# Performance work log

Measured on AMD Instinct MI355X. Metric: run time of the kernel, lower is better.

Reference implementation:

```python
import jax, jax.numpy as jnp
import numpy as np
import math

B, Q_LEN, PAST, HID = 1, 1024, 3072, 4096
NH, NKV, HD = 32, 8, 128
KV_LEN = PAST + Q_LEN
ROPE_THETA = 10000.0


def setup_inputs() -> dict:
    key = jax.random.key(0)
    ks = jax.random.split(key, 8)
    s = 0.02
    hidden_states = jax.random.normal(ks[0], (B, Q_LEN, HID), jnp.float32)
    # additive causal mask with KV cache offset: query i attends keys j <= PAST + i
    i = jnp.arange(Q_LEN)[:, None]
    j = jnp.arange(KV_LEN)[None, :]
    attention_mask = jnp.where(j <= PAST + i, 0.0, -1e9).astype(jnp.float32)[None, None]
    position_ids = (jnp.arange(Q_LEN, dtype=jnp.int64) + PAST)[None, :]
    past_k = jax.random.normal(ks[1], (B, NKV, PAST, HD), jnp.float32)
    past_v = jax.random.normal(ks[2], (B, NKV, PAST, HD), jnp.float32)
    Wq = jax.random.normal(ks[3], (NH * HD, HID), jnp.float32) * s
    Wk = jax.random.normal(ks[4], (NKV * HD, HID), jnp.float32) * s
    Wv = jax.random.normal(ks[5], (NKV * HD, HID), jnp.float32) * s
    Wo = jax.random.normal(ks[6], (HID, NH * HD), jnp.float32) * s
    return {"hidden_states": hidden_states, "attention_mask": attention_mask,
            "position_ids": position_ids, "past_k": past_k, "past_v": past_v,
            "Wq": Wq, "Wk": Wk, "Wv": Wv, "Wo": Wo}


def _rope_tables(seq_len, head_dim, dtype):
    inv_freq = 1.0 / (ROPE_THETA ** (jnp.arange(0, head_dim, 2, dtype=jnp.float32) / head_dim))
    t = jnp.arange(seq_len, dtype=jnp.float32)
    freqs = jnp.outer(t, inv_freq)            # [seq, hd/2]
    emb = jnp.concatenate([freqs, freqs], -1)  # [seq, hd]
    return jnp.cos(emb).astype(dtype), jnp.sin(emb).astype(dtype)


def _rotate_half(x):
    x1, x2 = jnp.split(x, 2, axis=-1)
    return jnp.concatenate([-x2, x1], axis=-1)


def reference(hidden_states, attention_mask, position_ids, past_k, past_v, Wq, Wk, Wv, Wo):
    bsz, q_len, _ = hidden_states.shape
    q = (hidden_states @ Wq.T).reshape(bsz, q_len, NH, HD).transpose(0, 2, 1, 3)
    k = (hidden_states @ Wk.T).reshape(bsz, q_len, NKV, HD).transpose(0, 2, 1, 3)
    v = (hidden_states @ Wv.T).reshape(bsz, q_len, NKV, HD).transpose(0, 2, 1, 3)

    kv_seq_len = q_len + past_k.shape[2]
    cos_t, sin_t = _rope_tables(kv_seq_len, HD, q.dtype)
    cos = cos_t[position_ids][:, None]  # [b,1,q,hd]
    sin = sin_t[position_ids][:, None]
    q = q * cos + _rotate_half(q) * sin
    k = k * cos + _rotate_half(k) * sin

    k = jnp.concatenate([past_k, k], axis=2)  # [b,nkv,kv,hd]
    v = jnp.concatenate([past_v, v], axis=2)
    n_rep = NH // NKV
    k = jnp.repeat(k, n_rep, axis=1)  # GQA repeat_kv -> [b,nh,kv,hd]
    v = jnp.repeat(v, n_rep, axis=1)

    scores = jnp.einsum('bhqd,bhkd->bhqk', q, k) / math.sqrt(HD)
    scores = scores + attention_mask
    weights = jax.nn.softmax(scores.astype(jnp.float32), axis=-1).astype(q.dtype)
    attn = jnp.einsum('bhqk,bhkd->bhqd', weights, v)
    attn = attn.transpose(0, 2, 1, 3).reshape(bsz, q_len, NH * HD)
    return attn @ Wo.T
```

## Files before the change

### kernel.cpp

```cpp
#include <hip/hip_runtime.h>

#define QLEN 1024
#define PASTN 3072
#define KVLEN 4096
#define HIDN 4096
#define NHEAD 32
#define NKVH 8
#define HDIM 128
#define NQKVC 6144

typedef unsigned short u16;
typedef __bf16 bf16x8 __attribute__((ext_vector_type(8)));
typedef float f32x4 __attribute__((ext_vector_type(4)));
typedef float f32x16 __attribute__((ext_vector_type(16)));
typedef u16 us8 __attribute__((ext_vector_type(8)));
typedef u16 us4 __attribute__((ext_vector_type(4)));

__device__ __forceinline__ u16 f2bf(float x) {
  unsigned u = __builtin_bit_cast(unsigned, x);
  u += 0x7fffu + ((u >> 16) & 1u);
  return (u16)(u >> 16);
}
__device__ __forceinline__ float bf2f(u16 b) {
  return __builtin_bit_cast(float, (unsigned)b << 16);
}

#define GLL16(gp, lp) __builtin_amdgcn_global_load_lds( \
    (const __attribute__((address_space(1))) void*)(gp), \
    (__attribute__((address_space(3))) void*)(lp), 16, 0, 0)

__global__ __launch_bounds__(256) void cvt5_kernel(const float* __restrict__ hid,
                                                   const float* __restrict__ wq,
                                                   const float* __restrict__ wk,
                                                   const float* __restrict__ wv,
                                                   const float* __restrict__ woin,
                                                   u16* __restrict__ hb,
                                                   u16* __restrict__ wb,
                                                   u16* __restrict__ wob) {
  const int blk = blockIdx.x;
  const float* src;
  u16* dst;
  int off;
  if (blk < 4096)       { src = hid;  dst = hb;                       off = blk; }
  else if (blk < 20480) { src = wq;   dst = wb;                       off = blk - 4096; }
  else if (blk < 24576) { src = wk;   dst = wb + (size_t)4096 * HIDN; off = blk - 20480; }
  else if (blk < 28672) { src = wv;   dst = wb + (size_t)5120 * HIDN; off = blk - 24576; }
  else                  { src = woin; dst = wob;                      off = blk - 28672; }
  const int i = off * 1024 + threadIdx.x * 4;
  float4 f = *(const float4*)(src + i);
  ushort4 o = make_ushort4(f2bf(f.x), f2bf(f.y), f2bf(f.z), f2bf(f.w));
  *(ushort4*)(dst + i) = o;
}

__device__ __forceinline__ void storeC(float* p, float v) { *p = v; }
__device__ __forceinline__ void storeC(u16* p, float v) { *p = f2bf(v); }

template <typename CT>
__global__ __launch_bounds__(256) void gemm_bt(const u16* __restrict__ A,
                                               const u16* __restrict__ B,
                                               CT* __restrict__ C, int M, int N, int K) {
  __shared__ u16 Alds[2][128 * 32];
  __shared__ u16 Blds[2][128 * 32];
  const int tid = threadIdx.x, wid = tid >> 6, lane = tid & 63;
  const int m0 = blockIdx.y * 128, n0 = blockIdx.x * 128;
  const int wm = (wid >> 1) * 64, wn = (wid & 1) * 64;
  const int l15 = lane & 15, l4 = lane >> 4;
  const int srow = lane >> 2;
  const int scol = ((lane & 3) ^ ((lane >> 3) & 3)) * 8;
  f32x4 acc[4][4] = {};
  auto stage = [&](int buf, int kt) {
#pragma unroll
    for (int i = 0; i < 2; ++i) {
      const int c = wid * 2 + i;
      const int row = c * 16 + srow;
      GLL16(A + (size_t)(m0 + row) * K + kt + scol, &Alds[buf][c * 512]);
      GLL16(B + (size_t)(n0 + row) * K + kt + scol, &Blds[buf][c * 512]);
    }
  };
  stage(0, 0);
  __syncthreads();
  int cur = 0;
  for (int kt = 0; kt < K; kt += 32) {
    if (kt + 32 < K) stage(cur ^ 1, kt + 32);
    bf16x8 a[4], b[4];
#pragma unroll
    for (int i = 0; i < 4; ++i) {
      const int R = wm + i * 16 + l15;
      const int slot = l4 ^ ((R >> 1) & 3);
      a[i] = *(const bf16x8*)&Alds[cur][R * 32 + slot * 8];
    }
#pragma unroll
    for (int j = 0; j < 4; ++j) {
      const int R = wn + j * 16 + l15;
      const int slot = l4 ^ ((R >> 1) & 3);
      b[j] = *(const bf16x8*)&Blds[cur][R * 32 + slot * 8];
    }
#pragma unroll
    for (int i = 0; i < 4; ++i)
#pragma unroll
      for (int j = 0; j < 4; ++j)
        acc[i][j] = __builtin_amdgcn_mfma_f32_16x16x32_bf16(a[i], b[j], acc[i][j], 0, 0, 0);
    __syncthreads();
    cur ^= 1;
  }
#pragma unroll
  for (int i = 0; i < 4; ++i)
#pragma unroll
    for (int j = 0; j < 4; ++j) {
      int row = m0 + wm + i * 16 + l4 * 4;
      int col = n0 + wn + j * 16 + l15;
#pragma unroll
      for (int r = 0; r < 4; ++r) storeC(&C[(size_t)(row + r) * N + col], acc[i][j][r]);
    }
}

__global__ __launch_bounds__(256) void rope_q_kernel(const u16* __restrict__ qkv,
                                                     u16* __restrict__ qr) {
  int idx = blockIdx.x * 256 + threadIdx.x;
  int i = idx & 63, h = (idx >> 6) & 31, r = idx >> 11;
  float freq = __expf(-(float)i * (9.210340371976184f / 64.f));
  float angle = (float)(PASTN + r) * freq;
  float sn, cs;
  sincosf(angle, &sn, &cs);
  int base = r * NQKVC + h * HDIM + i;
  float x1 = bf2f(qkv[base]);
  float x2 = bf2f(qkv[base + 64]);
  int ob = r * HIDN + h * HDIM + i;
  qr[ob] = f2bf(x1 * cs - x2 * sn);
  qr[ob + 64] = f2bf(x2 * cs + x1 * sn);
}

__global__ __launch_bounds__(256) void repack_k_kernel(const float* __restrict__ past_k,
                                                       const u16* __restrict__ qkv,
                                                       u16* __restrict__ kb) {
  int idx = blockIdx.x * 256 + threadIdx.x;
  int d = idx & 127, kv = (idx >> 7) & 4095, hk = idx >> 19;
  float val;
  if (kv < PASTN) {
    val = past_k[((size_t)hk * PASTN + kv) * HDIM + d];
  } else {
    int r = kv - PASTN;
    float x = bf2f(qkv[(size_t)r * NQKVC + 4096 + hk * HDIM + d]);
    float xp = bf2f(qkv[(size_t)r * NQKVC + 4096 + hk * HDIM + (d ^ 64)]);
    int i = d & 63;
    float freq = __expf(-(float)i * (9.210340371976184f / 64.f));
    float angle = (float)(PASTN + r) * freq;
    float sn, cs;
    sincosf(angle, &sn, &cs);
    val = (d < 64) ? (x * cs - xp * sn) : (x * cs + xp * sn);
  }
  kb[idx] = f2bf(val);
}

__global__ __launch_bounds__(256) void repack_vt_kernel(const float* __restrict__ past_v,
                                                        const u16* __restrict__ qkv,
                                                        u16* __restrict__ vtb) {
  __shared__ u16 tile[32][136];
  int hk = blockIdx.y, kv0 = blockIdx.x * 32, tid = threadIdx.x;
  int j = tid >> 3, d0 = (tid & 7) * 16;
  if (kv0 < PASTN) {
    const float* src = past_v + ((size_t)hk * PASTN + kv0 + j) * HDIM + d0;
#pragma unroll
    for (int x = 0; x < 16; x += 4) {
      float4 f = *(const float4*)(src + x);
      tile[j][d0 + x] = f2bf(f.x);
      tile[j][d0 + x + 1] = f2bf(f.y);
      tile[j][d0 + x + 2] = f2bf(f.z);
      tile[j][d0 + x + 3] = f2bf(f.w);
    }
  } else {
    int r = kv0 - PASTN + j;
    const u16* src = qkv + (size_t)r * NQKVC + 5120 + hk * HDIM + d0;
    *(us8*)&tile[j][d0] = *(const us8*)src;
    *(us8*)&tile[j][d0 + 8] = *(const us8*)(src + 8);
  }
  __syncthreads();
  int d = tid >> 1, jb = (tid & 1) * 16;
  us8 o0, o1;
#pragma unroll
  for (int x = 0; x < 8; ++x) {
    o0[x] = tile[jb + x][d];
    o1[x] = tile[jb + 8 + x][d];
  }
  u16* dst = vtb + ((size_t)hk * HDIM + d) * KVLEN + kv0 + jb;
  *(us8*)dst = o0;
  *(us8*)(dst + 8) = o1;
}

__global__ __launch_bounds__(512) void attn_kernel(const u16* __restrict__ q,
                                                   const u16* __restrict__ kc,
                                                   const u16* __restrict__ vt,
                                                   float* __restrict__ opart,
                                                   float* __restrict__ mlbuf) {
  __shared__ u16 Klds[2][64 * 128];
  __shared__ u16 Vlds[2][128 * 64];
  const int tid = threadIdx.x, wid = tid >> 6, lane = tid & 63;
  const int l31 = lane & 31, hi = lane >> 5, l15 = lane & 15;
  const int h = blockIdx.y, hk = h >> 2;
  const int q0 = blockIdx.x * 256;
  const int z = blockIdx.z;
  const int pid = h * 4 + blockIdx.x;
  const int qrow = q0 + wid * 32 + l31;
  bf16x8 qf[8];
  {
    const u16* qp = q + (size_t)qrow * HIDN + h * HDIM + hi * 8;
#pragma unroll
    for (int dk = 0; dk < 8; ++dk) qf[dk] = *(const bf16x8*)(qp + dk * 16);
  }
  float m_run = -1e30f, l_run = 0.f;
  f32x16 oacc[4] = {};
  const u16* kbase = kc + (size_t)hk * KVLEN * HDIM;
  const u16* vbase = vt + (size_t)hk * HDIM * KVLEN;
  const int ntiles = (PASTN + q0 + 256) >> 6;
  const int half = ntiles >> 1;
  const int t0 = z ? half : 0, t1 = z ? ntiles : half;
  const float C = 0.12753102f;
  const int qpos = PASTN + qrow;
  auto stage = [&](int buf, int kv0) {
#pragma unroll
    for (int i = 0; i < 2; ++i) {
      const int w = wid * 2 + i;
      const int p = w * 4 + (lane >> 4);
      const int key = (p & 0x33) | ((p & 4) << 1) | ((p & 8) >> 1);
      const int sl = (lane & 15) ^ (p & 15);
      GLL16(kbase + (size_t)(kv0 + key) * HDIM + sl * 8, &Klds[buf][w * 512]);
    }
#pragma unroll
    for (int i = 0; i < 2; ++i) {
      const int w = wid * 2 + i;
      const int d = w * 8 + (lane >> 3);
      const int sl = (lane & 7) ^ ((lane >> 3) & 7);
      GLL16(vbase + (size_t)d * KVLEN + kv0 + sl * 8, &Vlds[buf][w * 512]);
    }
  };
  stage(0, t0 << 6);
  __syncthreads();
  int cur = 0;
  for (int t = t0; t < t1; ++t) {
    if (t + 1 < t1) stage(cur ^ 1, (t + 1) << 6);
    const int kv0 = t << 6;
    const u16* Kb = Klds[cur];
    const u16* Vb = Vlds[cur];
    f32x16 s[2] = {};
    __builtin_amdgcn_s_setprio(1);
#pragma unroll
    for (int tt = 0; tt < 2; ++tt)
#pragma unroll
      for (int dk = 0; dk < 8; ++dk) {
        const int idx = (tt * 32 + l31) * 128 + (((dk * 2 + hi) ^ l15) * 8);
        bf16x8 kf = *(const bf16x8*)&Kb[idx];
        s[tt] = __builtin_amdgcn_mfma_f32_32x32x16_bf16(kf, qf[dk], s[tt], 0, 0, 0);
      }
    __builtin_amdgcn_s_setprio(0);
    float pm = -1e30f;
    if (kv0 + 63 > PASTN + q0) {
#pragma unroll
      for (int tt = 0; tt < 2; ++tt)
#pragma unroll
        for (int reg = 0; reg < 16; ++reg) {
          const int key = kv0 + tt * 32 + (reg & 7) + 8 * hi + ((reg & 8) << 1);
          float v = s[tt][reg] * C;
          if (key > qpos) v = -1e30f;
          s[tt][reg] = v;
          pm = fmaxf(pm, v);
        }
    } else {
#pragma unroll
      for (int tt = 0; tt < 2; ++tt)
#pragma unroll
        for (int reg = 0; reg < 16; ++reg) {
          float v = s[tt][reg] * C;
          s[tt][reg] = v;
          pm = fmaxf(pm, v);
        }
    }
    pm = fmaxf(pm, __shfl_xor(pm, 32));
    if (!__all(pm <= m_run)) {
      const float mn = fmaxf(m_run, pm);
      const float corr = exp2f(m_run - mn);
      m_run = mn;
      l_run *= corr;
#pragma unroll
      for (int db = 0; db < 4; ++db)
#pragma unroll
        for (int r = 0; r < 16; ++r) oacc[db][r] *= corr;
    }
    float rs = 0.f;
#pragma unroll
    for (int tt = 0; tt < 2; ++tt)
#pragma unroll
      for (int reg = 0; reg < 16; ++reg) {
        const float p = exp2f(s[tt][reg] - m_run);
        s[tt][reg] = p;
        rs += p;
      }
    rs += __shfl_xor(rs, 32);
    l_run += rs;
    __builtin_amdgcn_s_setprio(1);
#pragma unroll
    for (int kc2 = 0; kc2 < 4; ++kc2) {
      bf16x8 pa;
#pragma unroll
      for (int j = 0; j < 8; ++j) pa[j] = (__bf16)s[kc2 >> 1][(kc2 & 1) * 8 + j];
#pragma unroll
      for (int db = 0; db < 4; ++db) {
        const int idx = (db * 32 + l31) * 64 + (((kc2 * 2 + hi) ^ (l31 & 7)) * 8);
        bf16x8 vf = *(const bf16x8*)&Vb[idx];
        oacc[db] = __builtin_amdgcn_mfma_f32_32x32x16_bf16(vf, pa, oacc[db], 0, 0, 0);
      }
    }
    __builtin_amdgcn_s_setprio(0);
    __syncthreads();
    cur ^= 1;
  }
  const int orow = wid * 32 + l31;
  float* op = opart + ((size_t)(z * 128 + pid) * 256 + orow) * 128;
#pragma unroll
  for (int db = 0; db < 4; ++db)
#pragma unroll
    for (int g = 0; g < 4; ++g) {
      f32x4 w4;
#pragma unroll
      for (int j = 0; j < 4; ++j) w4[j] = oacc[db][g * 4 + j];
      *(f32x4*)&op[db * 32 + g * 8 + hi * 4] = w4;
    }
  if (hi == 0) {
    float* mlp = mlbuf + ((size_t)(z * 128 + pid) * 256 + orow) * 2;
    mlp[0] = m_run;
    mlp[1] = l_run;
  }
}

__global__ __launch_bounds__(256) void attn_combine(const float* __restrict__ opart,
                                                    const float* __restrict__ mlbuf,
                                                    u16* __restrict__ o) {
  const int pid = blockIdx.x;
  const int h = pid >> 2, qt = pid & 3;
  const int q2 = threadIdx.x >> 2, dc = (threadIdx.x & 3) * 32;
#pragma unroll
  for (int b = 0; b < 4; ++b) {
    const int q = b * 64 + q2;
    const float* ml0 = mlbuf + ((size_t)pid * 256 + q) * 2;
    const float* ml1 = mlbuf + ((size_t)(128 + pid) * 256 + q) * 2;
    const float m0 = ml0[0], l0 = ml0[1], m1 = ml1[0], l1 = ml1[1];
    const float m = fmaxf(m0, m1);
    const float w0 = exp2f(m0 - m), w1 = exp2f(m1 - m);
    const float inv = 1.f / (w0 * l0 + w1 * l1);
    const float* O0 = opart + ((size_t)pid * 256 + q) * 128 + dc;
    const float* O1 = opart + ((size_t)(128 + pid) * 256 + q) * 128 + dc;
    u16* dst = o + (size_t)(qt * 256 + q) * HIDN + h * HDIM + dc;
#pragma unroll
    for (int x = 0; x < 8; ++x) {
      f32x4 a = *(const f32x4*)(O0 + x * 4);
      f32x4 bb = *(const f32x4*)(O1 + x * 4);
      us4 w4;
#pragma unroll
      for (int j = 0; j < 4; ++j) w4[j] = f2bf((a[j] * w0 + bb[j] * w1) * inv);
      *(us4*)(dst + x * 4) = w4;
    }
  }
}

extern "C" void kernel_launch(void* const* d_in, const int* in_sizes, int n_in,
                              void* d_out, int out_size, void* d_ws, size_t ws_size,
                              hipStream_t stream) {
  (void)in_sizes; (void)n_in; (void)out_size; (void)ws_size;
  const float* hidden = (const float*)d_in[0];
  const float* past_k = (const float*)d_in[3];
  const float* past_v = (const float*)d_in[4];
  const float* Wq = (const float*)d_in[5];
  const float* Wk = (const float*)d_in[6];
  const float* Wv = (const float*)d_in[7];
  const float* Wo = (const float*)d_in[8];
  float* out = (float*)d_out;

  char* w = (char*)d_ws;
  u16* hiddenb = (u16*)w; w += (size_t)QLEN * HIDN * 2;
  u16* wqkv    = (u16*)w; w += (size_t)NQKVC * HIDN * 2;
  u16* wo      = (u16*)w; w += (size_t)HIDN * HIDN * 2;
  u16* qkvraw  = (u16*)w; w += (size_t)QLEN * NQKVC * 2;
  u16* qrope   = (u16*)w; w += (size_t)QLEN * HIDN * 2;
  u16* kbuf    = (u16*)w; w += (size_t)NKVH * KVLEN * HDIM * 2;
  u16* vtbuf   = (u16*)w; w += (size_t)NKVH * HDIM * KVLEN * 2;
  u16* attnb   = (u16*)w; w += (size_t)QLEN * HIDN * 2;
  float* opart = (float*)wqkv;
  float* mlbuf = opart + (size_t)2 * 128 * 256 * 128;

  cvt5_kernel<<<45056, 256, 0, stream>>>(hidden, Wq, Wk, Wv, Wo, hiddenb, wqkv, wo);

  gemm_bt<u16><<<dim3(NQKVC / 128, QLEN / 128), 256, 0, stream>>>(hiddenb, wqkv, qkvraw,
                                                                  QLEN, NQKVC, HIDN);

  rope_q_kernel<<<(QLEN * NHEAD * 64) / 256, 256, 0, stream>>>(qkvraw, qrope);
  repack_k_kernel<<<(NKVH * KVLEN * HDIM) / 256, 256, 0, stream>>>(past_k, qkvraw, kbuf);
  repack_vt_kernel<<<dim3(KVLEN / 32, NKVH), 256, 0, stream>>>(past_v, qkvraw, vtbuf);

  attn_kernel<<<dim3(QLEN / 256, NHEAD, 2), 512, 0, stream>>>(qrope, kbuf, vtbuf,
                                                              opart, mlbuf);
  attn_combine<<<128, 256, 0, stream>>>(opart, mlbuf, attnb);

  gemm_bt<float><<<dim3(HIDN / 128, QLEN / 128), 256, 0, stream>>>(attnb, wo, out,
                                                                   QLEN, HIDN, HIDN);
}
```

Before: 347.8 us.

## Triple-buffer GEMM LDS staging with partial vmcnt waits

The bf16 GEMM moves from a double-buffered to a triple-buffered LDS pipeline, prefetching two K-tiles ahead. Each iteration waits only on the older tile's global-to-LDS loads (vmcnt(4)) instead of draining all of them with __syncthreads, so more memory latency can overlap the MFMAs. In exchange LDS use per block goes up by half, which may lower occupancy, and the hand-written waitcnt and barrier sequence is fragile if the number of loads per stage changes.

```diff
diff --git a/kernel.cpp b/kernel.cpp
--- a/kernel.cpp
+++ b/kernel.cpp
@@ -59,8 +59,8 @@
 __global__ __launch_bounds__(256) void gemm_bt(const u16* __restrict__ A,
                                                const u16* __restrict__ B,
                                                CT* __restrict__ C, int M, int N, int K) {
-  __shared__ u16 Alds[2][128 * 32];
-  __shared__ u16 Blds[2][128 * 32];
+  __shared__ u16 Alds[3][128 * 32];
+  __shared__ u16 Blds[3][128 * 32];
   const int tid = threadIdx.x, wid = tid >> 6, lane = tid & 63;
   const int m0 = blockIdx.y * 128, n0 = blockIdx.x * 128;
   const int wm = (wid >> 1) * 64, wn = (wid & 1) * 64;
@@ -77,31 +77,44 @@
       GLL16(B + (size_t)(n0 + row) * K + kt + scol, &Blds[buf][c * 512]);
     }
   };
+  const int NT = K >> 5;
   stage(0, 0);
-  __syncthreads();
+  stage(1, 32);
+  asm volatile("s_waitcnt vmcnt(4) lgkmcnt(0)" ::: "memory");
+  __builtin_amdgcn_s_barrier();
+  __builtin_amdgcn_sched_barrier(0);
   int cur = 0;
-  for (int kt = 0; kt < K; kt += 32) {
-    if (kt + 32 < K) stage(cur ^ 1, kt + 32);
+  for (int t = 0; t < NT; ++t) {
+    int s2 = cur + 2; if (s2 >= 3) s2 -= 3;
+    if (t + 2 < NT) stage(s2, (t + 2) << 5);
+    const u16* Ab = &Alds[cur][0];
+    const u16* Bb = &Blds[cur][0];
     bf16x8 a[4], b[4];
 #pragma unroll
     for (int i = 0; i < 4; ++i) {
       const int R = wm + i * 16 + l15;
-      const int slot = l4 ^ ((R >> 1) & 3);
-      a[i] = *(const bf16x8*)&Alds[cur][R * 32 + slot * 8];
+      a[i] = *(const bf16x8*)&Ab[R * 32 + (l4 ^ ((R >> 1) & 3)) * 8];
     }
 #pragma unroll
     for (int j = 0; j < 4; ++j) {
       const int R = wn + j * 16 + l15;
-      const int slot = l4 ^ ((R >> 1) & 3);
-      b[j] = *(const bf16x8*)&Blds[cur][R * 32 + slot * 8];
+      b[j] = *(const bf16x8*)&Bb[R * 32 + (l4 ^ ((R >> 1) & 3)) * 8];
     }
 #pragma unroll
     for (int i = 0; i < 4; ++i)
 #pragma unroll
       for (int j = 0; j < 4; ++j)
         acc[i][j] = __builtin_amdgcn_mfma_f32_16x16x32_bf16(a[i], b[j], acc[i][j], 0, 0, 0);
-    __syncthreads();
-    cur ^= 1;
+    if (t + 2 < NT) {
+      asm volatile("s_waitcnt vmcnt(4) lgkmcnt(0)" ::: "memory");
+      __builtin_amdgcn_s_barrier();
+      __builtin_amdgcn_sched_barrier(0);
+    } else if (t + 1 < NT) {
+      asm volatile("s_waitcnt vmcnt(0) lgkmcnt(0)" ::: "memory");
+      __builtin_amdgcn_s_barrier();
+      __builtin_amdgcn_sched_barrier(0);
+    }
+    cur += 1; if (cur >= 3) cur -= 3;
   }
 #pragma unroll
   for (int i = 0; i < 4; ++i)
```

Result: no change. 353.2 us (+1.5%).
